# Optimization experiments

Measured on AMD Instinct MI355X. Metric: run time of the kernel, lower is better.

## Reference

```python
import jax, jax.numpy as jnp
import numpy as np

N_NODES = 100000


def _gcn_norm(edge_index, num_nodes):
    """Add self-loops and compute symmetric GCN normalization coeffs.
    Returns (row, col, norm) with self-loops appended."""
    loops = jnp.arange(num_nodes, dtype=edge_index.dtype)
    row = jnp.concatenate([edge_index[0], loops])
    col = jnp.concatenate([edge_index[1], loops])
    ones = jnp.ones(row.shape[0], dtype=jnp.float32)
    deg = jax.ops.segment_sum(ones, col, num_segments=num_nodes)
    dinv = jnp.where(deg > 0, jax.lax.rsqrt(deg), 0.0)
    norm = dinv[row] * dinv[col]  # [E + N]
    return row, col, norm


def _gcn_conv(x, W, b, row, col, norm, num_nodes):
    h = x @ W                      # [N, out] dense GEMM first (PyG order)
    msg = h[row] * norm[:, None]   # gather + scale per edge
    agg = jax.ops.segment_sum(msg, col, num_segments=num_nodes)
    return agg + b


def setup_inputs() -> dict:
    key = jax.random.key(0)
    k1, k2, k3, k4 = jax.random.split(key, 4)
    x = jax.random.normal(k1, (N_NODES, 500), dtype=jnp.float32)
    W1 = jax.random.normal(k2, (500, 128), dtype=jnp.float32) * (1.0 / np.sqrt(500))
    b1 = jnp.zeros((128,), dtype=jnp.float32)
    W2 = jax.random.normal(k3, (128, 64), dtype=jnp.float32) * (1.0 / np.sqrt(128))
    b2 = jnp.zeros((64,), dtype=jnp.float32)
    edge_index = jax.random.randint(k4, (2, 3200000), 0, N_NODES, dtype=jnp.int32)
    return {"x": x, "W1": W1, "b1": b1, "W2": W2, "b2": b2,
            "edge_index": edge_index}


def reference(x, W1, b1, W2, b2, edge_index):
    num_nodes = x.shape[0]
    row, col, norm = _gcn_norm(edge_index, num_nodes)
    # encode (dropout is identity in eval mode)
    h = _gcn_conv(x, W1, b1, row, col, norm, num_nodes)
    h = jax.nn.relu(h)
    z = _gcn_conv(h, W2, b2, row, col, norm, num_nodes)
    # decode: per-edge dot product of endpoint embeddings
    scores = jnp.sum(z[edge_index[0]] * z[edge_index[1]], axis=1)  # [E]
    return scores
```

## Files before the change

kernel.cpp:

```cpp
#include <hip/hip_runtime.h>

#define NN 100000
#define K1 500
#define F1 128
#define F2 64

#define NBLK   128
#define BSH    7
#define NBUCK  ((NN + 127) >> 7)
#define NBUCKP 784
#define CAP    6144

typedef __attribute__((ext_vector_type(8))) short short8;
typedef __attribute__((ext_vector_type(4))) float floatx4;
typedef __attribute__((ext_vector_type(4))) unsigned int uintx4;

static __device__ __forceinline__ unsigned short f2bf(float f) {
    unsigned int u = __float_as_uint(f);
    unsigned int r = (u + 0x7FFF + ((u >> 16) & 1)) >> 16;
    return (unsigned short)r;
}
static __device__ __forceinline__ void bf2x(unsigned int u, float& lo, float& hi) {
    lo = __uint_as_float(u << 16);
    hi = __uint_as_float(u & 0xffff0000u);
}
static __device__ __forceinline__ unsigned int cvtpk(float lo, float hi) {
    unsigned int r;
    asm("v_cvt_pk_bf16_f32 %0, %1, %2" : "=v"(r) : "v"(lo), "v"(hi));
    return r;
}

typedef __attribute__((address_space(3))) unsigned int u32_lds;
typedef const __attribute__((address_space(1))) unsigned int u32_g;
static __device__ __forceinline__ void stage16(const float* g, float* l) {
    __builtin_amdgcn_global_load_lds((u32_g*)g, (u32_lds*)l, 16, 0, 0);
}

__global__ __launch_bounds__(256) void k_pa(const int* __restrict__ col, int E, int chunk,
                                            int* __restrict__ HT) {
    __shared__ int hist[NBUCKP];
    for (int i = threadIdx.x; i < NBUCKP; i += 256) hist[i] = 0;
    __syncthreads();
    const int b = blockIdx.x;
    const int s = b * chunk;
    const int e0 = min(E, s + chunk);
    for (int e = s + threadIdx.x; e < e0; e += 256)
        atomicAdd(&hist[col[e] >> BSH], 1);
    __syncthreads();
    for (int i = threadIdx.x; i < NBUCK; i += 256)
        HT[i * NBLK + b] = hist[i];
}

__global__ __launch_bounds__(128) void k_bsum(const int* __restrict__ HT, int* __restrict__ S) {
    __shared__ int s[128];
    const int tid = threadIdx.x;
    s[tid] = HT[blockIdx.x * NBLK + tid];
    __syncthreads();
    for (int off = 64; off; off >>= 1) {
        if (tid < off) s[tid] += s[tid + off];
        __syncthreads();
    }
    if (tid == 0) S[blockIdx.x] = s[0];
}

__global__ __launch_bounds__(1024) void k_bscan(const int* __restrict__ S,
                                                int* __restrict__ BB, int nb, int E) {
    __shared__ int s[1024];
    const int tid = threadIdx.x;
    int v = (tid < nb) ? S[tid] : 0;
    s[tid] = v;
    __syncthreads();
    for (int off = 1; off < 1024; off <<= 1) {
        int t = (tid >= off) ? s[tid - off] : 0;
        __syncthreads();
        s[tid] += t;
        __syncthreads();
    }
    if (tid < nb) BB[tid] = s[tid] - v;
    if (tid == 0) BB[nb] = E;
}

__global__ __launch_bounds__(128) void k_boff(int* __restrict__ HT, const int* __restrict__ BB) {
    __shared__ int s[128];
    const int tid = threadIdx.x;
    const int rowb = blockIdx.x * NBLK;
    int v = HT[rowb + tid];
    s[tid] = v;
    __syncthreads();
    for (int off = 1; off < 128; off <<= 1) {
        int t = (tid >= off) ? s[tid - off] : 0;
        __syncthreads();
        s[tid] += t;
        __syncthreads();
    }
    HT[rowb + tid] = s[tid] - v + BB[blockIdx.x];
}

__global__ __launch_bounds__(256) void k_pc(const int* __restrict__ row,
                                            const int* __restrict__ col, int E, int chunk,
                                            const int* __restrict__ HT,
                                            unsigned long long* __restrict__ pairs) {
    __shared__ int cur[NBUCKP];
    const int b = blockIdx.x;
    for (int i = threadIdx.x; i < NBUCK; i += 256) cur[i] = HT[i * NBLK + b];
    __syncthreads();
    const int s = b * chunk;
    const int e0 = min(E, s + chunk);
    for (int e = s + threadIdx.x; e < e0; e += 256) {
        const int r = row[e], c = col[e];
        const int p = atomicAdd(&cur[c >> BSH], 1);
        pairs[p] = ((unsigned long long)(unsigned)c << 32) | (unsigned)r;
    }
}

__global__ __launch_bounds__(256) void k_pd(const unsigned long long* __restrict__ pairs,
                                            const int* __restrict__ BB,
                                            int* __restrict__ ptr, float* __restrict__ dinv,
                                            int* __restrict__ idx) {
    __shared__ int colcnt[128], colptr[128], cur[128];
    __shared__ int lidx[CAP];
    const int buck = blockIdx.x;
    const int base = BB[buck];
    int count = BB[buck + 1] - base;
    if (count > CAP) count = CAP;
    const int lo = buck << BSH;
    const int tid = threadIdx.x;
    if (tid < 128) colcnt[tid] = 0;
    __syncthreads();
    for (int e = tid; e < count; e += 256) {
        const int c = (int)(pairs[base + e] >> 32);
        atomicAdd(&colcnt[c & 127], 1);
    }
    __syncthreads();
    if (tid < 128) colptr[tid] = colcnt[tid];
    __syncthreads();
    for (int off = 1; off < 128; off <<= 1) {
        int t = 0;
        if (tid < 128 && tid >= off) t = colptr[tid - off];
        __syncthreads();
        if (tid < 128) colptr[tid] += t;
        __syncthreads();
    }
    if (tid < 128) {
        const int excl = colptr[tid] - colcnt[tid];
        cur[tid] = excl;
        const int c = lo + tid;
        if (c < NN) {
            ptr[c]  = base + excl;
            dinv[c] = rsqrtf((float)colcnt[tid] + 1.0f);
        }
    }
    __syncthreads();
    for (int e = tid; e < count; e += 256) {
        const unsigned long long pr = pairs[base + e];
        const int c = (int)(pr >> 32);
        const int p = atomicAdd(&cur[c & 127], 1);
        lidx[p] = (int)(pr & 0xffffffffu);
    }
    __syncthreads();
    for (int e = tid; e < count; e += 256)
        idx[base + e] = lidx[e];
}

__global__ __launch_bounds__(256) void k_w1t(const float* __restrict__ W1,
                                             unsigned short* __restrict__ W1T) {
    int t = blockIdx.x * 256 + threadIdx.x;
    int n = t >> 9, k = t & 511;
    W1T[t] = (k < K1) ? f2bf(W1[k * F1 + n]) : (unsigned short)0;
}

__global__ __launch_bounds__(256, 2) void k_gemm1_mfma(
    const float* __restrict__ x,
    const unsigned short* __restrict__ W1T,
    const float* __restrict__ dinv,
    unsigned short* __restrict__ h)
{
    __shared__ __align__(16) float xs[32 * 512];
    const int tid  = threadIdx.x;
    const int wave = tid >> 6;
    const int lane = tid & 63;
    const int q    = lane >> 4;
    const int m16  = lane & 15;
    const int blkRow  = blockIdx.x * 32;
    const int colBase = wave * 32;

    short8 bw[2][16];
#pragma unroll
    for (int nt = 0; nt < 2; ++nt)
#pragma unroll
        for (int t = 0; t < 16; ++t)
            bw[nt][t] = *(const short8*)(W1T + (colBase + nt * 16 + m16) * 512 + t * 32 + q * 8);

#pragma unroll
    for (int i = 0; i < 16; ++i) {
        const int s = i * 256 + tid;
        const int r = s >> 7;
        const int c = s & 127;
        int cs = c ^ (r & 7);
        if (cs > 124) cs = 124;
        const float* src = x + (size_t)(blkRow + r) * K1 + cs * 4;
        stage16(src, xs + (size_t)s * 4);
    }
    __syncthreads();

    floatx4 acc[2][2];
#pragma unroll
    for (int mt = 0; mt < 2; ++mt)
#pragma unroll
        for (int nt = 0; nt < 2; ++nt) acc[mt][nt] = (floatx4){0.f, 0.f, 0.f, 0.f};

#pragma unroll
    for (int t = 0; t < 16; ++t) {
        short8 afr[2];
#pragma unroll
        for (int mt = 0; mt < 2; ++mt) {
            const int rr = mt * 16 + m16;
            const int c0 = t * 8 + (( 2 * q )     ^ (rr & 7));
            const int c1 = t * 8 + (( 2 * q + 1 ) ^ (rr & 7));
            const floatx4 v0 = *(const floatx4*)(xs + rr * 512 + c0 * 4);
            const floatx4 v1 = *(const floatx4*)(xs + rr * 512 + c1 * 4);
            uintx4 p;
            p[0] = cvtpk(v0[0], v0[1]);
            p[1] = cvtpk(v0[2], v0[3]);
            p[2] = cvtpk(v1[0], v1[1]);
            p[3] = cvtpk(v1[2], v1[3]);
            afr[mt] = __builtin_bit_cast(short8, p);
        }
#pragma unroll
        for (int mt = 0; mt < 2; ++mt)
#pragma unroll
            for (int nt = 0; nt < 2; ++nt)
                acc[mt][nt] = __builtin_amdgcn_mfma_f32_16x16x32_bf16(
                    afr[mt], bw[nt][t], acc[mt][nt], 0, 0, 0);
    }

#pragma unroll
    for (int mt = 0; mt < 2; ++mt) {
        const int rbase = blkRow + mt * 16 + q * 4;
#pragma unroll
        for (int r = 0; r < 4; ++r) {
            const int row = rbase + r;
            const float dr = dinv[row];
#pragma unroll
            for (int nt = 0; nt < 2; ++nt)
                h[(size_t)row * F1 + colBase + nt * 16 + m16] = f2bf(acc[mt][nt][r] * dr);
        }
    }
}

__global__ __launch_bounds__(256) void k_agg1(const int* __restrict__ ptr,
                                              const int* __restrict__ idx, int E,
                                              const float* __restrict__ dinv,
                                              const unsigned short* __restrict__ h,
                                              float* __restrict__ agg) {
    const int c    = blockIdx.x * 4 + (threadIdx.x >> 6);
    const int lane = threadIdx.x & 63;
    const int es = lane >> 3, fg = lane & 7;
    float acc[16];
#pragma unroll
    for (int j = 0; j < 16; ++j) acc[j] = 0.f;
    if (es == 0) {
        const uint4 u0 = *(const uint4*)(h + (size_t)c * F1 + fg * 16);
        const uint4 u1 = *(const uint4*)(h + (size_t)c * F1 + fg * 16 + 8);
        bf2x(u0.x, acc[0], acc[1]);  bf2x(u0.y, acc[2], acc[3]);
        bf2x(u0.z, acc[4], acc[5]);  bf2x(u0.w, acc[6], acc[7]);
        bf2x(u1.x, acc[8], acc[9]);  bf2x(u1.y, acc[10], acc[11]);
        bf2x(u1.z, acc[12], acc[13]); bf2x(u1.w, acc[14], acc[15]);
    }
    const int s   = ptr[c];
    const int end = (c + 1 < NN) ? ptr[c + 1] : E;
    int e = s + es;
    for (; e + 8 < end; e += 16) {
        const int r0 = idx[e], r1 = idx[e + 8];
        const uint4 u00 = *(const uint4*)(h + (size_t)r0 * F1 + fg * 16);
        const uint4 u01 = *(const uint4*)(h + (size_t)r0 * F1 + fg * 16 + 8);
        const uint4 u10 = *(const uint4*)(h + (size_t)r1 * F1 + fg * 16);
        const uint4 u11 = *(const uint4*)(h + (size_t)r1 * F1 + fg * 16 + 8);
        float lo, hi;
        bf2x(u00.x, lo, hi); acc[0] += lo; acc[1] += hi;
        bf2x(u00.y, lo, hi); acc[2] += lo; acc[3] += hi;
        bf2x(u00.z, lo, hi); acc[4] += lo; acc[5] += hi;
        bf2x(u00.w, lo, hi); acc[6] += lo; acc[7] += hi;
        bf2x(u01.x, lo, hi); acc[8] += lo; acc[9] += hi;
        bf2x(u01.y, lo, hi); acc[10] += lo; acc[11] += hi;
        bf2x(u01.z, lo, hi); acc[12] += lo; acc[13] += hi;
        bf2x(u01.w, lo, hi); acc[14] += lo; acc[15] += hi;
        bf2x(u10.x, lo, hi); acc[0] += lo; acc[1] += hi;
        bf2x(u10.y, lo, hi); acc[2] += lo; acc[3] += hi;
        bf2x(u10.z, lo, hi); acc[4] += lo; acc[5] += hi;
        bf2x(u10.w, lo, hi); acc[6] += lo; acc[7] += hi;
        bf2x(u11.x, lo, hi); acc[8] += lo; acc[9] += hi;
        bf2x(u11.y, lo, hi); acc[10] += lo; acc[11] += hi;
        bf2x(u11.z, lo, hi); acc[12] += lo; acc[13] += hi;
        bf2x(u11.w, lo, hi); acc[14] += lo; acc[15] += hi;
    }
    if (e < end) {
        const int r = idx[e];
        const uint4 u0 = *(const uint4*)(h + (size_t)r * F1 + fg * 16);
        const uint4 u1 = *(const uint4*)(h + (size_t)r * F1 + fg * 16 + 8);
        float lo, hi;
        bf2x(u0.x, lo, hi); acc[0] += lo; acc[1] += hi;
        bf2x(u0.y, lo, hi); acc[2] += lo; acc[3] += hi;
        bf2x(u0.z, lo, hi); acc[4] += lo; acc[5] += hi;
        bf2x(u0.w, lo, hi); acc[6] += lo; acc[7] += hi;
        bf2x(u1.x, lo, hi); acc[8] += lo; acc[9] += hi;
        bf2x(u1.y, lo, hi); acc[10] += lo; acc[11] += hi;
        bf2x(u1.z, lo, hi); acc[12] += lo; acc[13] += hi;
        bf2x(u1.w, lo, hi); acc[14] += lo; acc[15] += hi;
    }
#pragma unroll
    for (int j = 0; j < 16; ++j) {
        acc[j] += __shfl_xor(acc[j], 8);
        acc[j] += __shfl_xor(acc[j], 16);
        acc[j] += __shfl_xor(acc[j], 32);
    }
    if (es == 0) {
        const float dc = dinv[c];
        float* o = agg + (size_t)c * F1 + fg * 16;
        float4 o0 = {acc[0] * dc, acc[1] * dc, acc[2] * dc, acc[3] * dc};
        float4 o1 = {acc[4] * dc, acc[5] * dc, acc[6] * dc, acc[7] * dc};
        float4 o2 = {acc[8] * dc, acc[9] * dc, acc[10] * dc, acc[11] * dc};
        float4 o3 = {acc[12] * dc, acc[13] * dc, acc[14] * dc, acc[15] * dc};
        *(float4*)(o)      = o0;
        *(float4*)(o + 4)  = o1;
        *(float4*)(o + 8)  = o2;
        *(float4*)(o + 12) = o3;
    }
}

__global__ __launch_bounds__(256) void k_gemm2(const float* __restrict__ agg1,
                                               const float* __restrict__ b1,
                                               const float* __restrict__ W2,
                                               const float* __restrict__ dinv,
                                               unsigned short* __restrict__ h2) {
    __shared__ __align__(16) float W2s[F1 * F2];
    __shared__ __align__(16) float xs[64 * F1];
    const int tid = threadIdx.x;
    const int r0  = blockIdx.x * 64;
    for (int i = tid; i < F1 * F2; i += 256) W2s[i] = W2[i];
    const int base = r0 * F1;
    for (int i = tid; i < 64 * F1; i += 256) {
        int gi = base + i;
        float v = 0.f;
        if (gi < NN * F1) v = fmaxf(agg1[gi] + b1[i & (F1 - 1)], 0.f);
        xs[i] = v;
    }
    __syncthreads();

    const int j = tid & 63;
    const int g = tid >> 6;
    float acc[16];
#pragma unroll
    for (int rr = 0; rr < 16; ++rr) acc[rr] = 0.f;

    for (int k = 0; k < F1; k += 4) {
        const float w0 = W2s[(k + 0) * F2 + j];
        const float w1 = W2s[(k + 1) * F2 + j];
        const float w2 = W2s[(k + 2) * F2 + j];
        const float w3 = W2s[(k + 3) * F2 + j];
#pragma unroll
        for (int rr = 0; rr < 16; ++rr) {
            const float4 xv = *(const float4*)&xs[(g * 16 + rr) * F1 + k];
            acc[rr] += xv.x * w0 + xv.y * w1 + xv.z * w2 + xv.w * w3;
        }
    }
#pragma unroll
    for (int rr = 0; rr < 16; ++rr) {
        int r = r0 + g * 16 + rr;
        if (r < NN) h2[(size_t)r * F2 + j] = f2bf(acc[rr] * dinv[r]);
    }
}

__global__ __launch_bounds__(256) void k_agg2(const int* __restrict__ ptr,
                                              const int* __restrict__ idx, int E,
                                              const float* __restrict__ dinv,
                                              const unsigned short* __restrict__ h2,
                                              const float* __restrict__ b2,
                                              unsigned short* __restrict__ z) {
    const int c    = blockIdx.x * 4 + (threadIdx.x >> 6);
    const int lane = threadIdx.x & 63;
    const int es = lane >> 3, fg = lane & 7;
    float a[8];
#pragma unroll
    for (int j = 0; j < 8; ++j) a[j] = 0.f;
    if (es == 0) {
        const uint4 u = *(const uint4*)(h2 + (size_t)c * F2 + fg * 8);
        bf2x(u.x, a[0], a[1]); bf2x(u.y, a[2], a[3]);
        bf2x(u.z, a[4], a[5]); bf2x(u.w, a[6], a[7]);
    }
    const int s   = ptr[c];
    const int end = (c + 1 < NN) ? ptr[c + 1] : E;
    int e = s + es;
    for (; e + 8 < end; e += 16) {
        const int r0 = idx[e], r1 = idx[e + 8];
        const uint4 u0 = *(const uint4*)(h2 + (size_t)r0 * F2 + fg * 8);
        const uint4 u1 = *(const uint4*)(h2 + (size_t)r1 * F2 + fg * 8);
        float lo, hi;
        bf2x(u0.x, lo, hi); a[0] += lo; a[1] += hi;
        bf2x(u0.y, lo, hi); a[2] += lo; a[3] += hi;
        bf2x(u0.z, lo, hi); a[4] += lo; a[5] += hi;
        bf2x(u0.w, lo, hi); a[6] += lo; a[7] += hi;
        bf2x(u1.x, lo, hi); a[0] += lo; a[1] += hi;
        bf2x(u1.y, lo, hi); a[2] += lo; a[3] += hi;
        bf2x(u1.z, lo, hi); a[4] += lo; a[5] += hi;
        bf2x(u1.w, lo, hi); a[6] += lo; a[7] += hi;
    }
    if (e < end) {
        const int r = idx[e];
        const uint4 u = *(const uint4*)(h2 + (size_t)r * F2 + fg * 8);
        float lo, hi;
        bf2x(u.x, lo, hi); a[0] += lo; a[1] += hi;
        bf2x(u.y, lo, hi); a[2] += lo; a[3] += hi;
        bf2x(u.z, lo, hi); a[4] += lo; a[5] += hi;
        bf2x(u.w, lo, hi); a[6] += lo; a[7] += hi;
    }
#pragma unroll
    for (int j = 0; j < 8; ++j) {
        a[j] += __shfl_xor(a[j], 8);
        a[j] += __shfl_xor(a[j], 16);
        a[j] += __shfl_xor(a[j], 32);
    }
    if (es == 0) {
        const float dc = dinv[c];
        const float4 b0 = *(const float4*)(b2 + fg * 8);
        const float4 b1v = *(const float4*)(b2 + fg * 8 + 4);
        uint4 o;
        o.x = (unsigned)f2bf(a[0] * dc + b0.x)  | ((unsigned)f2bf(a[1] * dc + b0.y)  << 16);
        o.y = (unsigned)f2bf(a[2] * dc + b0.z)  | ((unsigned)f2bf(a[3] * dc + b0.w)  << 16);
        o.z = (unsigned)f2bf(a[4] * dc + b1v.x) | ((unsigned)f2bf(a[5] * dc + b1v.y) << 16);
        o.w = (unsigned)f2bf(a[6] * dc + b1v.z) | ((unsigned)f2bf(a[7] * dc + b1v.w) << 16);
        *(uint4*)(z + (size_t)c * F2 + fg * 8) = o;
    }
}

__global__ void k_decode(const int* __restrict__ src, const int* __restrict__ dst,
                         int E, const unsigned short* __restrict__ z,
                         float* __restrict__ out) {
    long t = (long)blockIdx.x * blockDim.x + threadIdx.x;
    int e = (int)(t >> 3);
    int l = (int)(t & 7);
    if (e >= E) return;
    const int s = src[e], d = dst[e];
    const uint4 us = *(const uint4*)(z + (size_t)s * F2 + l * 8);
    const uint4 ud = *(const uint4*)(z + (size_t)d * F2 + l * 8);
    float sl, sh, dl, dh;
    float v;
    bf2x(us.x, sl, sh); bf2x(ud.x, dl, dh); v  = sl * dl + sh * dh;
    bf2x(us.y, sl, sh); bf2x(ud.y, dl, dh); v += sl * dl + sh * dh;
    bf2x(us.z, sl, sh); bf2x(ud.z, dl, dh); v += sl * dl + sh * dh;
    bf2x(us.w, sl, sh); bf2x(ud.w, dl, dh); v += sl * dl + sh * dh;
    v += __shfl_down(v, 4, 8);
    v += __shfl_down(v, 2, 8);
    v += __shfl_down(v, 1, 8);
    if (l == 0) out[e] = v;
}

extern "C" void kernel_launch(void* const* d_in, const int* in_sizes, int n_in,
                              void* d_out, int out_size, void* d_ws, size_t ws_size,
                              hipStream_t stream) {
    const float* x  = (const float*)d_in[0];
    const float* W1 = (const float*)d_in[1];
    const float* b1 = (const float*)d_in[2];
    const float* W2 = (const float*)d_in[3];
    const float* b2 = (const float*)d_in[4];
    const int*   ei = (const int*)d_in[5];
    const int E = in_sizes[5] / 2;
    const int* rowp = ei;
    const int* colp = ei + E;

    char* wsb = (char*)d_ws;
    float* dinv = (float*)wsb;                 wsb += 100352 * 4;
    int*   ptr  = (int*)wsb;                   wsb += 100352 * 4;
    int*   S    = (int*)wsb;                   wsb += 1024 * 4;
    int*   BB   = (int*)wsb;                   wsb += 1024 * 4;
    int*   HT   = (int*)wsb;                   wsb += (size_t)1024 * NBLK * 4;
    int*   idx  = (int*)wsb;                   wsb += (size_t)E * 4;
    unsigned short* W1T = (unsigned short*)wsb; wsb += 128 * 512 * 2;
    unsigned short* hbf = (unsigned short*)wsb; wsb += (size_t)NN * F1 * 2;
    float* agg1 = (float*)wsb;                 wsb += (size_t)NN * F1 * 4;
    unsigned short* h2 = (unsigned short*)wsb; wsb += (size_t)NN * F2 * 2;
    unsigned long long* pairs = (unsigned long long*)agg1;
    unsigned short* z = hbf;
    float* out  = (float*)d_out;

    const int chunk = (E + NBLK - 1) / NBLK;

    k_pa   <<<NBLK, 256, 0, stream>>>(colp, E, chunk, HT);
    k_bsum <<<NBUCK, 128, 0, stream>>>(HT, S);
    k_bscan<<<1, 1024, 0, stream>>>(S, BB, NBUCK, E);
    k_boff <<<NBUCK, 128, 0, stream>>>(HT, BB);
    k_pc   <<<NBLK, 256, 0, stream>>>(rowp, colp, E, chunk, HT, pairs);
    k_pd   <<<NBUCK, 256, 0, stream>>>(pairs, BB, ptr, dinv, idx);

    k_w1t<<<256, 256, 0, stream>>>(W1, W1T);
    k_gemm1_mfma<<<NN / 32, 256, 0, stream>>>(x, W1T, dinv, hbf);
    k_agg1<<<NN / 4, 256, 0, stream>>>(ptr, idx, E, dinv, hbf, agg1);

    k_gemm2<<<(NN + 63) / 64, 256, 0, stream>>>(agg1, b1, W2, dinv, h2);
    k_agg2<<<NN / 4, 256, 0, stream>>>(ptr, idx, E, dinv, h2, b2, z);

    const long dthreads = (long)E * 8;
    k_decode<<<(int)((dthreads + 255) / 256), 256, 0, stream>>>(
        rowp, colp, E, z, out);
}
```

Measured before the change: 790.9 us.

## Decode edge scores per destination node using CSR order and original edge ids

The 64-bit sort key now packs column, row and original edge index, and k_pd emits a second array, eidx, that maps each CSR slot back to its original edge. The decode kernel now runs one wave per destination node. Each wave loads that node's z vector once into registers, walks its incoming edges to gather only the source embedding, and scatters the score to out[eidx]. This halves the random z gathers per edge. In exchange it adds an extra E-sized index array write and read, doubles the LDS used in k_pd, and replaces coalesced output stores with scattered 4-byte writes.

Measured after the change: 817.9 us. 1.03x slower.

```diff
diff --git a/kernel.cpp b/kernel.cpp
--- a/kernel.cpp
+++ b/kernel.cpp
@@ -10,6 +10,11 @@
 #define NBUCK  ((NN + 127) >> 7)
 #define NBUCKP 784
 #define CAP    6144
+
+#define PSH_C  39
+#define PSH_R  22
+#define PM_R   0x1FFFF
+#define PM_E   0x3FFFFF
 
 typedef __attribute__((ext_vector_type(8))) short short8;
 typedef __attribute__((ext_vector_type(4))) float floatx4;
@@ -109,16 +114,19 @@
     for (int e = s + threadIdx.x; e < e0; e += 256) {
         const int r = row[e], c = col[e];
         const int p = atomicAdd(&cur[c >> BSH], 1);
-        pairs[p] = ((unsigned long long)(unsigned)c << 32) | (unsigned)r;
+        pairs[p] = ((unsigned long long)(unsigned)c << PSH_C)
+                 | ((unsigned long long)(unsigned)r << PSH_R)
+                 | (unsigned)e;
     }
 }
 
 __global__ __launch_bounds__(256) void k_pd(const unsigned long long* __restrict__ pairs,
                                             const int* __restrict__ BB,
                                             int* __restrict__ ptr, float* __restrict__ dinv,
-                                            int* __restrict__ idx) {
+                                            int* __restrict__ idx, int* __restrict__ eidx) {
     __shared__ int colcnt[128], colptr[128], cur[128];
     __shared__ int lidx[CAP];
+    __shared__ int leid[CAP];
     const int buck = blockIdx.x;
     const int base = BB[buck];
     int count = BB[buck + 1] - base;
@@ -128,7 +136,7 @@
     if (tid < 128) colcnt[tid] = 0;
     __syncthreads();
     for (int e = tid; e < count; e += 256) {
-        const int c = (int)(pairs[base + e] >> 32);
+        const int c = (int)(pairs[base + e] >> PSH_C);
         atomicAdd(&colcnt[c & 127], 1);
     }
     __syncthreads();
@@ -153,13 +161,16 @@
     __syncthreads();
     for (int e = tid; e < count; e += 256) {
         const unsigned long long pr = pairs[base + e];
-        const int c = (int)(pr >> 32);
+        const int c = (int)(pr >> PSH_C);
         const int p = atomicAdd(&cur[c & 127], 1);
-        lidx[p] = (int)(pr & 0xffffffffu);
-    }
-    __syncthreads();
-    for (int e = tid; e < count; e += 256)
-        idx[base + e] = lidx[e];
+        lidx[p] = (int)((pr >> PSH_R) & PM_R);
+        leid[p] = (int)(pr & PM_E);
+    }
+    __syncthreads();
+    for (int e = tid; e < count; e += 256) {
+        idx[base + e]  = lidx[e];
+        eidx[base + e] = leid[e];
+    }
 }
 
 __global__ __launch_bounds__(256) void k_w1t(const float* __restrict__ W1,
@@ -433,26 +444,54 @@
     }
 }
 
-__global__ void k_decode(const int* __restrict__ src, const int* __restrict__ dst,
-                         int E, const unsigned short* __restrict__ z,
-                         float* __restrict__ out) {
-    long t = (long)blockIdx.x * blockDim.x + threadIdx.x;
-    int e = (int)(t >> 3);
-    int l = (int)(t & 7);
-    if (e >= E) return;
-    const int s = src[e], d = dst[e];
-    const uint4 us = *(const uint4*)(z + (size_t)s * F2 + l * 8);
-    const uint4 ud = *(const uint4*)(z + (size_t)d * F2 + l * 8);
-    float sl, sh, dl, dh;
-    float v;
-    bf2x(us.x, sl, sh); bf2x(ud.x, dl, dh); v  = sl * dl + sh * dh;
-    bf2x(us.y, sl, sh); bf2x(ud.y, dl, dh); v += sl * dl + sh * dh;
-    bf2x(us.z, sl, sh); bf2x(ud.z, dl, dh); v += sl * dl + sh * dh;
-    bf2x(us.w, sl, sh); bf2x(ud.w, dl, dh); v += sl * dl + sh * dh;
-    v += __shfl_down(v, 4, 8);
-    v += __shfl_down(v, 2, 8);
-    v += __shfl_down(v, 1, 8);
-    if (l == 0) out[e] = v;
+__global__ __launch_bounds__(256) void k_decode(const int* __restrict__ ptr,
+                                                const int* __restrict__ idx,
+                                                const int* __restrict__ eidx, int E,
+                                                const unsigned short* __restrict__ z,
+                                                float* __restrict__ out) {
+    const int c    = blockIdx.x * 4 + (threadIdx.x >> 6);
+    const int lane = threadIdx.x & 63;
+    const int es = lane >> 3, fg = lane & 7;
+    const uint4 uc = *(const uint4*)(z + (size_t)c * F2 + fg * 8);
+    float c0, c1, c2, c3, c4, c5, c6, c7;
+    bf2x(uc.x, c0, c1); bf2x(uc.y, c2, c3);
+    bf2x(uc.z, c4, c5); bf2x(uc.w, c6, c7);
+    const int s   = ptr[c];
+    const int end = (c + 1 < NN) ? ptr[c + 1] : E;
+    int e = s + es;
+    for (; e + 8 < end; e += 16) {
+        const int r0 = idx[e],  r1 = idx[e + 8];
+        const int i0 = eidx[e], i1 = eidx[e + 8];
+        const uint4 u0 = *(const uint4*)(z + (size_t)r0 * F2 + fg * 8);
+        const uint4 u1 = *(const uint4*)(z + (size_t)r1 * F2 + fg * 8);
+        float lo, hi, v0, v1;
+        bf2x(u0.x, lo, hi); v0  = lo * c0 + hi * c1;
+        bf2x(u0.y, lo, hi); v0 += lo * c2 + hi * c3;
+        bf2x(u0.z, lo, hi); v0 += lo * c4 + hi * c5;
+        bf2x(u0.w, lo, hi); v0 += lo * c6 + hi * c7;
+        bf2x(u1.x, lo, hi); v1  = lo * c0 + hi * c1;
+        bf2x(u1.y, lo, hi); v1 += lo * c2 + hi * c3;
+        bf2x(u1.z, lo, hi); v1 += lo * c4 + hi * c5;
+        bf2x(u1.w, lo, hi); v1 += lo * c6 + hi * c7;
+        v0 += __shfl_xor(v0, 1); v1 += __shfl_xor(v1, 1);
+        v0 += __shfl_xor(v0, 2); v1 += __shfl_xor(v1, 2);
+        v0 += __shfl_xor(v0, 4); v1 += __shfl_xor(v1, 4);
+        if (fg == 0) { out[i0] = v0; out[i1] = v1; }
+    }
+    if (e < end) {
+        const int r = idx[e];
+        const int i = eidx[e];
+        const uint4 u = *(const uint4*)(z + (size_t)r * F2 + fg * 8);
+        float lo, hi, v;
+        bf2x(u.x, lo, hi); v  = lo * c0 + hi * c1;
+        bf2x(u.y, lo, hi); v += lo * c2 + hi * c3;
+        bf2x(u.z, lo, hi); v += lo * c4 + hi * c5;
+        bf2x(u.w, lo, hi); v += lo * c6 + hi * c7;
+        v += __shfl_xor(v, 1);
+        v += __shfl_xor(v, 2);
+        v += __shfl_xor(v, 4);
+        if (fg == 0) out[i] = v;
+    }
 }
 
 extern "C" void kernel_launch(void* const* d_in, const int* in_sizes, int n_in,
@@ -475,6 +514,7 @@
     int*   BB   = (int*)wsb;                   wsb += 1024 * 4;
     int*   HT   = (int*)wsb;                   wsb += (size_t)1024 * NBLK * 4;
     int*   idx  = (int*)wsb;                   wsb += (size_t)E * 4;
+    int*   eidx = (int*)wsb;                   wsb += (size_t)E * 4;
     unsigned short* W1T = (unsigned short*)wsb; wsb += 128 * 512 * 2;
     unsigned short* hbf = (unsigned short*)wsb; wsb += (size_t)NN * F1 * 2;
     float* agg1 = (float*)wsb;                 wsb += (size_t)NN * F1 * 4;
@@ -490,7 +530,7 @@
     k_bscan<<<1, 1024, 0, stream>>>(S, BB, NBUCK, E);
     k_boff <<<NBUCK, 128, 0, stream>>>(HT, BB);
     k_pc   <<<NBLK, 256, 0, stream>>>(rowp, colp, E, chunk, HT, pairs);
-    k_pd   <<<NBUCK, 256, 0, stream>>>(pairs, BB, ptr, dinv, idx);
+    k_pd   <<<NBUCK, 256, 0, stream>>>(pairs, BB, ptr, dinv, idx, eidx);
 
     k_w1t<<<256, 256, 0, stream>>>(W1, W1T);
     k_gemm1_mfma<<<NN / 32, 256, 0, stream>>>(x, W1T, dinv, hbf);
@@ -499,7 +539,5 @@
     k_gemm2<<<(NN + 63) / 64, 256, 0, stream>>>(agg1, b1, W2, dinv, h2);
     k_agg2<<<NN / 4, 256, 0, stream>>>(ptr, idx, E, dinv, h2, b2, z);
 
-    const long dthreads = (long)E * 8;
-    k_decode<<<(int)((dthreads + 255) / 256), 256, 0, stream>>>(
-        rowp, colp, E, z, out);
-}
+    k_decode<<<NN / 4, 256, 0, stream>>>(ptr, idx, eidx, E, z, out);
+}
```

## Fuse layer-1 aggregation with the second GEMM into one kernel

Applied to the files above, without the earlier changes.

The layer-1 neighbour aggregation now applies bias and ReLU in registers. Each wave then computes its node's 64-wide h2 row directly from a W2 copy held in shared memory. This removes the fp32 agg1 intermediate (written once and read back), the separate gemm2 launch, and the agg1 allocation, so the edge-pair buffer gets its own workspace slot. In exchange, every 4-node block reloads the full 32 KB W2 into LDS, adding a large amount of repeated L2 traffic. The larger LDS footprint may also lower occupancy for the latency-bound gather loop.

Result: no change. 791.8 us (+0.1%).

```diff
diff --git a/kernel.cpp b/kernel.cpp
--- a/kernel.cpp
+++ b/kernel.cpp
@@ -248,14 +248,23 @@
     }
 }
 
-__global__ __launch_bounds__(256) void k_agg1(const int* __restrict__ ptr,
-                                              const int* __restrict__ idx, int E,
-                                              const float* __restrict__ dinv,
-                                              const unsigned short* __restrict__ h,
-                                              float* __restrict__ agg) {
-    const int c    = blockIdx.x * 4 + (threadIdx.x >> 6);
-    const int lane = threadIdx.x & 63;
+__global__ __launch_bounds__(256) void k_agg1g2(
+    const int* __restrict__ ptr, const int* __restrict__ idx, int E,
+    const float* __restrict__ dinv, const unsigned short* __restrict__ h,
+    const float* __restrict__ b1, const float* __restrict__ W2,
+    unsigned short* __restrict__ h2)
+{
+    __shared__ __align__(16) float W2s[F1 * F2];
+    __shared__ __align__(16) float xrow[4][F1];
+    const int tid  = threadIdx.x;
+    const int wave = tid >> 6;
+    const int lane = tid & 63;
     const int es = lane >> 3, fg = lane & 7;
+
+    for (int i = tid; i < F1 * F2; i += 256) W2s[i] = W2[i];
+    __syncthreads();
+
+    const int c = blockIdx.x * 4 + wave;
     float acc[16];
 #pragma unroll
     for (int j = 0; j < 16; ++j) acc[j] = 0.f;
@@ -314,61 +323,25 @@
         acc[j] += __shfl_xor(acc[j], 16);
         acc[j] += __shfl_xor(acc[j], 32);
     }
+    const float dc = dinv[c];
     if (es == 0) {
-        const float dc = dinv[c];
-        float* o = agg + (size_t)c * F1 + fg * 16;
-        float4 o0 = {acc[0] * dc, acc[1] * dc, acc[2] * dc, acc[3] * dc};
-        float4 o1 = {acc[4] * dc, acc[5] * dc, acc[6] * dc, acc[7] * dc};
-        float4 o2 = {acc[8] * dc, acc[9] * dc, acc[10] * dc, acc[11] * dc};
-        float4 o3 = {acc[12] * dc, acc[13] * dc, acc[14] * dc, acc[15] * dc};
-        *(float4*)(o)      = o0;
-        *(float4*)(o + 4)  = o1;
-        *(float4*)(o + 8)  = o2;
-        *(float4*)(o + 12) = o3;
-    }
-}
-
-__global__ __launch_bounds__(256) void k_gemm2(const float* __restrict__ agg1,
-                                               const float* __restrict__ b1,
-                                               const float* __restrict__ W2,
-                                               const float* __restrict__ dinv,
-                                               unsigned short* __restrict__ h2) {
-    __shared__ __align__(16) float W2s[F1 * F2];
-    __shared__ __align__(16) float xs[64 * F1];
-    const int tid = threadIdx.x;
-    const int r0  = blockIdx.x * 64;
-    for (int i = tid; i < F1 * F2; i += 256) W2s[i] = W2[i];
-    const int base = r0 * F1;
-    for (int i = tid; i < 64 * F1; i += 256) {
-        int gi = base + i;
-        float v = 0.f;
-        if (gi < NN * F1) v = fmaxf(agg1[gi] + b1[i & (F1 - 1)], 0.f);
-        xs[i] = v;
-    }
-    __syncthreads();
-
-    const int j = tid & 63;
-    const int g = tid >> 6;
-    float acc[16];
-#pragma unroll
-    for (int rr = 0; rr < 16; ++rr) acc[rr] = 0.f;
-
+        const float* bb = b1 + fg * 16;
+        float* xw = &xrow[wave][fg * 16];
+#pragma unroll
+        for (int j = 0; j < 16; ++j)
+            xw[j] = fmaxf(acc[j] * dc + bb[j], 0.f);
+    }
+
+    float h2a = 0.f;
+    const float* xr = xrow[wave];
     for (int k = 0; k < F1; k += 4) {
-        const float w0 = W2s[(k + 0) * F2 + j];
-        const float w1 = W2s[(k + 1) * F2 + j];
-        const float w2 = W2s[(k + 2) * F2 + j];
-        const float w3 = W2s[(k + 3) * F2 + j];
-#pragma unroll
-        for (int rr = 0; rr < 16; ++rr) {
-            const float4 xv = *(const float4*)&xs[(g * 16 + rr) * F1 + k];
-            acc[rr] += xv.x * w0 + xv.y * w1 + xv.z * w2 + xv.w * w3;
-        }
-    }
-#pragma unroll
-    for (int rr = 0; rr < 16; ++rr) {
-        int r = r0 + g * 16 + rr;
-        if (r < NN) h2[(size_t)r * F2 + j] = f2bf(acc[rr] * dinv[r]);
-    }
+        const float4 xv = *(const float4*)&xr[k];
+        h2a += xv.x * W2s[(k + 0) * F2 + lane]
+             + xv.y * W2s[(k + 1) * F2 + lane]
+             + xv.z * W2s[(k + 2) * F2 + lane]
+             + xv.w * W2s[(k + 3) * F2 + lane];
+    }
+    h2[(size_t)c * F2 + lane] = f2bf(h2a * dc);
 }
 
 __global__ __launch_bounds__(256) void k_agg2(const int* __restrict__ ptr,
@@ -477,9 +450,8 @@
     int*   idx  = (int*)wsb;                   wsb += (size_t)E * 4;
     unsigned short* W1T = (unsigned short*)wsb; wsb += 128 * 512 * 2;
     unsigned short* hbf = (unsigned short*)wsb; wsb += (size_t)NN * F1 * 2;
-    float* agg1 = (float*)wsb;                 wsb += (size_t)NN * F1 * 4;
     unsigned short* h2 = (unsigned short*)wsb; wsb += (size_t)NN * F2 * 2;
-    unsigned long long* pairs = (unsigned long long*)agg1;
+    unsigned long long* pairs = (unsigned long long*)wsb; wsb += (size_t)E * 8;
     unsigned short* z = hbf;
     float* out  = (float*)d_out;
 
@@ -494,9 +466,9 @@
 
     k_w1t<<<256, 256, 0, stream>>>(W1, W1T);
     k_gemm1_mfma<<<NN / 32, 256, 0, stream>>>(x, W1T, dinv, hbf);
-    k_agg1<<<NN / 4, 256, 0, stream>>>(ptr, idx, E, dinv, hbf, agg1);
-
-    k_gemm2<<<(NN + 63) / 64, 256, 0, stream>>>(agg1, b1, W2, dinv, h2);
+
+    k_agg1g2<<<NN / 4, 256, 0, stream>>>(ptr, idx, E, dinv, hbf, b1, W2, h2);
+
     k_agg2<<<NN / 4, 256, 0, stream>>>(ptr, idx, E, dinv, h2, b2, z);
 
     const long dthreads = (long)E * 8;
```
